# Kernel tuning notes

Measured on AMD Instinct MI355X. Metric: run time of the kernel, lower is better.

Reference implementation:

```python
import jax, jax.numpy as jnp
import numpy as np

B, T, D, H, O = 8, 16384, 256, 256, 256


def setup_inputs() -> dict:
    key = jax.random.key(0)
    ks = jax.random.split(key, 7)
    lim_d = 1.0 / np.sqrt(D)
    lim_h = 1.0 / np.sqrt(H)
    u = lambda k, shape, lim: jax.random.uniform(k, shape, jnp.float32, -lim, lim)
    return {
        "xs": jax.random.normal(ks[0], (B, T, D), jnp.float32),
        "Wz": u(ks[1], (H, D), lim_d),
        "bz": u(ks[2], (H,), lim_d),
        "Wh": u(ks[3], (H, D), lim_d),
        "bh": u(ks[4], (H,), lim_d),
        "Wo": u(ks[5], (O, H), lim_h),
        "bo": u(ks[6], (O,), lim_h),
    }


def reference(xs, Wz, bz, Wh, bh, Wo, bo):
    # gates and candidate hidden states (eqx.nn.Linear: y = W @ x + b)
    zs = jax.nn.sigmoid(jnp.einsum("btd,hd->bth", xs, Wz) + bz)  # [B,T,H]
    hs = jnp.einsum("btd,hd->bth", xs, Wh) + bh                  # [B,T,H]

    # prepend_ones / prepend_zeros along the time axis
    a = jnp.concatenate([jnp.ones_like(zs[:, :1]), 1.0 - zs], axis=1)    # [B,T+1,H]
    b = jnp.concatenate([jnp.zeros_like(zs[:, :1]), zs * hs], axis=1)    # [B,T+1,H]

    def combine(first, second):
        a0, b0 = first
        a1, b1 = second
        return (a0 * b0, b0 * a1 + b1)

    _, states = jax.lax.associative_scan(combine, (a, b), axis=1)
    return jnp.einsum("bth,oh->bto", states[:, 1:], Wo) + bo  # [B,T,O]
```

## Files before the change

### kernel.cpp

```cpp
#include <hip/hip_runtime.h>
#include <hip/hip_bf16.h>

#define Bsz 8
#define Tsz 16384
#define NL0 16385
#define NL5 512
#define NL10 16

typedef __attribute__((ext_vector_type(2))) float f32x2;
typedef __attribute__((ext_vector_type(4))) float f32x4;
typedef __attribute__((ext_vector_type(8))) short bf16x8;

__device__ __forceinline__ short f2bf(float f) {
  unsigned u = __builtin_bit_cast(unsigned, f);
  u += 0x7FFFu + ((u >> 16) & 1u);
  return (short)(u >> 16);
}
__device__ __forceinline__ unsigned cvtpk(float lo, float hi) {
  __hip_bfloat162 t = __float22bfloat162_rn(float2{lo, hi});
  unsigned u;
  __builtin_memcpy(&u, &t, 4);
  return u;
}
__device__ __forceinline__ bf16x8 pack8(f32x4 a, f32x4 b) {
  union { unsigned u[4]; bf16x8 v; } r;
  r.u[0] = cvtpk(a[0], a[1]); r.u[1] = cvtpk(a[2], a[3]);
  r.u[2] = cvtpk(b[0], b[1]); r.u[3] = cvtpk(b[2], b[3]);
  return r.v;
}
__device__ __forceinline__ void unpk(unsigned u, float& a, float& b) {
  a = __builtin_bit_cast(float, u << 16);
  b = __builtin_bit_cast(float, u & 0xFFFF0000u);
}

__global__ void fill_sentinel(float* __restrict__ out, int n) {
  int i = blockIdx.x * blockDim.x + threadIdx.x;
  if (i < n) out[i] = 12345.0f;
}

__global__ void prep_weights(const float* __restrict__ Wz, const float* __restrict__ Wh,
                             const float* __restrict__ Wo, unsigned short* __restrict__ wt) {
  int idx = blockIdx.x * 256 + threadIdx.x;
  if (idx >= 3 * 256 * 32) return;
  int m   = idx >> 13;
  int rem = idx & 8191;
  int r   = rem >> 5;
  int cq  = rem & 31;
  const float* src = (m == 0 ? Wz : (m == 1 ? Wh : Wo)) + r * 256 + cq * 8;
  f32x4 v0 = *(const f32x4*)src;
  f32x4 v1 = *(const f32x4*)(src + 4);
  *(bf16x8*)(wt + m * 65536 + (cq * 256 + r) * 8) = pack8(v0, v1);
}

__global__ void init_e0(unsigned* __restrict__ l0) {
  int idx = blockIdx.x * 256 + threadIdx.x;
  if (idx >= Bsz * 256) return;
  int batch = idx >> 8, h = idx & 255;
  l0[(size_t)batch * NL0 * 256 + h] = 0x00003F80u;
}

__global__ __launch_bounds__(512, 3)
void gemm_zh(const float* __restrict__ xs, const unsigned short* __restrict__ wt,
             const float* __restrict__ bz, const float* __restrict__ bh,
             unsigned* __restrict__ l0)
{
  __shared__ __align__(16) unsigned short aL[2][4096];

  const int tid = threadIdx.x;
  const int wave = tid >> 6, lane = tid & 63, l15 = lane & 15, l4 = lane >> 4;
  const int rowBase = blockIdx.x * 64;
  const int srow = tid & 63, soct = tid >> 6;
  const float* aptr = xs + (size_t)(rowBase + srow) * 256 + soct * 8;
  const unsigned short* wz_t = wt;
  const unsigned short* wh_t = wt + 65536;
  const int wn = wave * 32;

  f32x4 accz[4][2] = {};
  f32x4 acch[4][2] = {};

  f32x4 av0 = __builtin_nontemporal_load((const f32x4*)aptr);
  f32x4 av1 = __builtin_nontemporal_load((const f32x4*)(aptr + 4));
  *(bf16x8*)&aL[0][(soct * 64 + srow) * 8] = pack8(av0, av1);

  bf16x8 zc[2], hc[2], zn[2], hn[2];
#pragma unroll
  for (int n = 0; n < 2; ++n) {
    const int r = wn + n * 16 + l15;
    zc[n] = *(const bf16x8*)(wz_t + (l4 * 256 + r) * 8);
    hc[n] = *(const bf16x8*)(wh_t + (l4 * 256 + r) * 8);
  }

#pragma unroll
  for (int kk = 0; kk < 8; ++kk) {
    const int S = kk >> 1;
    if ((kk & 1) == 0) {
      __syncthreads();
      if (S < 3) {
        av0 = __builtin_nontemporal_load((const f32x4*)(aptr + (S + 1) * 64));
        av1 = __builtin_nontemporal_load((const f32x4*)(aptr + (S + 1) * 64 + 4));
      }
    }
    if (kk < 7) {
      const int cq = (kk + 1) * 4 + l4;
#pragma unroll
      for (int n = 0; n < 2; ++n) {
        const int r = wn + n * 16 + l15;
        zn[n] = *(const bf16x8*)(wz_t + (cq * 256 + r) * 8);
        hn[n] = *(const bf16x8*)(wh_t + (cq * 256 + r) * 8);
      }
    }
    bf16x8 af[4];
#pragma unroll
    for (int m = 0; m < 4; ++m)
      af[m] = *(const bf16x8*)&aL[S & 1][(((kk & 1) * 4 + l4) * 64 + m * 16 + l15) * 8];
#pragma unroll
    for (int m = 0; m < 4; ++m)
#pragma unroll
      for (int n = 0; n < 2; ++n) {
        accz[m][n] = __builtin_amdgcn_mfma_f32_16x16x32_bf16(af[m], zc[n], accz[m][n], 0, 0, 0);
        acch[m][n] = __builtin_amdgcn_mfma_f32_16x16x32_bf16(af[m], hc[n], acch[m][n], 0, 0, 0);
      }
    if ((kk & 1) && S < 3)
      *(bf16x8*)&aL[(S & 1) ^ 1][(soct * 64 + srow) * 8] = pack8(av0, av1);
    if (kk < 7) {
      zc[0] = zn[0]; zc[1] = zn[1];
      hc[0] = hn[0]; hc[1] = hn[1];
    }
  }

  const int batch = rowBase >> 14;
  const int tRow  = rowBase & (Tsz - 1);
#pragma unroll
  for (int n = 0; n < 2; ++n) {
    const int col = wn + n * 16 + l15;
    const float bzv = bz[col], bhv = bh[col];
#pragma unroll
    for (int m = 0; m < 4; ++m)
#pragma unroll
      for (int j = 0; j < 4; ++j) {
        const int t = tRow + m * 16 + l4 * 4 + j;
        const float zv = 1.0f / (1.0f + __expf(-(accz[m][n][j] + bzv)));
        const float hv = acch[m][n][j] + bhv;
        l0[((size_t)batch * NL0 + t + 1) * 256 + col] = cvtpk(1.0f - zv, zv * hv);
      }
  }
}

__global__ __launch_bounds__(256)
void chunk_up_bf16(const unsigned* __restrict__ l0, f32x2* __restrict__ dst)
{
  int idx = blockIdx.x * 256 + threadIdx.x;
  int h2 = idx & 127, r = idx >> 7;
  int c = r & 511, batch = r >> 9;
  size_t base = ((size_t)batch * NL0 + (size_t)c * 32) * 256 + h2 * 2;

  float ax[16], bx[16], ay[16], by[16];
#pragma unroll
  for (int i = 0; i < 16; ++i) {
    uint2 e0 = *(const uint2*)(l0 + base + (size_t)(2 * i) * 256);
    uint2 e1 = *(const uint2*)(l0 + base + (size_t)(2 * i + 1) * 256);
    float a0, b0, a1, b1;
    unpk(e0.x, a0, b0); unpk(e1.x, a1, b1);
    ax[i] = a0 * b0; bx[i] = b0 * a1 + b1;
    unpk(e0.y, a0, b0); unpk(e1.y, a1, b1);
    ay[i] = a0 * b0; by[i] = b0 * a1 + b1;
  }
#pragma unroll
  for (int n = 8; n >= 1; n >>= 1) {
#pragma unroll
    for (int i = 0; i < n; ++i) {
      float nax = ax[2*i] * bx[2*i], nbx = bx[2*i] * ax[2*i+1] + bx[2*i+1];
      float nay = ay[2*i] * by[2*i], nby = by[2*i] * ay[2*i+1] + by[2*i+1];
      ax[i] = nax; bx[i] = nbx; ay[i] = nay; by[i] = nby;
    }
  }
  f32x4 o = {ax[0], bx[0], ay[0], by[0]};
  *(f32x4*)((float*)dst + (((size_t)batch * 512 + c) * 256 + h2 * 2) * 2) = o;
}

__global__ __launch_bounds__(256)
void chunk_up(const f32x2* __restrict__ src, f32x2* __restrict__ dst, int nCh, int nSrc)
{
  int idx = blockIdx.x * 256 + threadIdx.x;
  int total = Bsz * nCh * 256;
  if (idx >= total) return;
  int h = idx & 255, r = idx >> 8;
  int c = r % nCh, batch = r / nCh;
  size_t base = ((size_t)batch * nSrc + (size_t)c * 32) * 256 + h;

  float a1[16], b1[16];
#pragma unroll
  for (int i = 0; i < 16; ++i) {
    f32x2 e0 = src[base + (size_t)(2 * i) * 256];
    f32x2 e1 = src[base + (size_t)(2 * i + 1) * 256];
    a1[i] = e0[0] * e0[1];
    b1[i] = e0[1] * e1[0] + e1[1];
  }
#pragma unroll
  for (int n = 8; n >= 1; n >>= 1) {
#pragma unroll
    for (int i = 0; i < n; ++i) {
      float na = a1[2 * i] * b1[2 * i];
      float nb = b1[2 * i] * a1[2 * i + 1] + b1[2 * i + 1];
      a1[i] = na; b1[i] = nb;
    }
  }
  dst[((size_t)batch * nCh + c) * 256 + h] = f32x2{a1[0], b1[0]};
}

__global__ void tree16(const f32x2* __restrict__ src, float* __restrict__ outB)
{
  int idx = blockIdx.x * 256 + threadIdx.x;
  if (idx >= Bsz * 256) return;
  int h = idx & 255, batch = idx >> 8;
  size_t base = (size_t)batch * 16 * 256 + h;

  float a0[16], b0[16];
#pragma unroll
  for (int i = 0; i < 16; ++i) { f32x2 e = src[base + (size_t)i * 256]; a0[i] = e[0]; b0[i] = e[1]; }
  float a1[8], b1[8];
#pragma unroll
  for (int i = 0; i < 8; ++i) { a1[i] = a0[2*i]*b0[2*i]; b1[i] = b0[2*i]*a0[2*i+1] + b0[2*i+1]; }
  float a2[4], b2[4];
#pragma unroll
  for (int i = 0; i < 4; ++i) { a2[i] = a1[2*i]*b1[2*i]; b2[i] = b1[2*i]*a1[2*i+1] + b1[2*i+1]; }
  float a3[2], b3[2];
#pragma unroll
  for (int i = 0; i < 2; ++i) { a3[i] = a2[2*i]*b2[2*i]; b3[i] = b2[2*i]*a2[2*i+1] + b2[2*i+1]; }
  float s3[2];
  s3[0] = b3[0];
  s3[1] = b3[0] * a3[1] + b3[1];
  float s2[4];
  s2[0] = b2[0]; s2[1] = s3[0]; s2[2] = s3[0] * a2[2] + b2[2]; s2[3] = s3[1];
  float s1[8];
  s1[0] = b1[0];
#pragma unroll
  for (int j = 0; j < 4; ++j) s1[2*j+1] = s2[j];
#pragma unroll
  for (int j = 1; j < 4; ++j) s1[2*j] = s2[j-1] * a1[2*j] + b1[2*j];
  float s0[16];
  s0[0] = b0[0];
#pragma unroll
  for (int j = 0; j < 8; ++j) s0[2*j+1] = s1[j];
#pragma unroll
  for (int j = 1; j < 8; ++j) s0[2*j] = s1[j-1] * a0[2*j] + b0[2*j];
#pragma unroll
  for (int i = 0; i < 16; ++i) outB[base + (size_t)i * 256] = s0[i];
}

__global__ __launch_bounds__(256, 2)
void chunk_down_f32(const f32x2* __restrict__ src, const float* __restrict__ snext,
                    float* __restrict__ outF, int nCh, int nFull, int nSrc)
{
  int idx = blockIdx.x * 256 + threadIdx.x;
  int total = Bsz * nCh * 256;
  if (idx >= total) return;
  int h = idx & 255, r = idx >> 8;
  int c = r % nCh, batch = r / nCh;
  size_t base = ((size_t)batch * nSrc + (size_t)c * 32) * 256 + h;
  bool hasP = (c > 0);
  float P = hasP ? snext[((size_t)batch * nFull + (c - 1)) * 256 + h] : 0.0f;
  float S = snext[((size_t)batch * nFull + c) * 256 + h];

  float ae[16], be[16], a1[16], b1[16];
#pragma unroll
  for (int i = 0; i < 16; ++i) {
    f32x2 e0 = src[base + (size_t)(2 * i) * 256];
    f32x2 e1 = src[base + (size_t)(2 * i + 1) * 256];
    ae[i] = e0[0]; be[i] = e0[1];
    a1[i] = e0[0] * e0[1];
    b1[i] = e0[1] * e1[0] + e1[1];
  }
  float a2[8], b2[8];
#pragma unroll
  for (int i = 0; i < 8; ++i) { a2[i] = a1[2*i]*b1[2*i]; b2[i] = b1[2*i]*a1[2*i+1] + b1[2*i+1]; }
  float a3[4], b3[4];
#pragma unroll
  for (int i = 0; i < 4; ++i) { a3[i] = a2[2*i]*b2[2*i]; b3[i] = b2[2*i]*a2[2*i+1] + b2[2*i+1]; }
  float a4[2], b4[2];
#pragma unroll
  for (int i = 0; i < 2; ++i) { a4[i] = a3[2*i]*b3[2*i]; b4[i] = b3[2*i]*a3[2*i+1] + b3[2*i+1]; }

  float s4[2];
  s4[0] = hasP ? P * a4[0] + b4[0] : b4[0];
  s4[1] = S;
  float s3[4];
  s3[0] = hasP ? P * a3[0] + b3[0] : b3[0];
  s3[1] = s4[0]; s3[2] = s4[0] * a3[2] + b3[2]; s3[3] = s4[1];
  float s2[8];
  s2[0] = hasP ? P * a2[0] + b2[0] : b2[0];
#pragma unroll
  for (int j = 0; j < 4; ++j) s2[2*j+1] = s3[j];
#pragma unroll
  for (int j = 1; j < 4; ++j) s2[2*j] = s3[j-1] * a2[2*j] + b2[2*j];
  float s1[16];
  s1[0] = hasP ? P * a1[0] + b1[0] : b1[0];
#pragma unroll
  for (int j = 0; j < 8; ++j) s1[2*j+1] = s2[j];
#pragma unroll
  for (int j = 1; j < 8; ++j) s1[2*j] = s2[j-1] * a1[2*j] + b1[2*j];

  outF[base] = hasP ? P * ae[0] + be[0] : be[0];
#pragma unroll
  for (int j = 0; j < 16; ++j) outF[base + (size_t)(2*j+1) * 256] = s1[j];
#pragma unroll
  for (int j = 1; j < 16; ++j) outF[base + (size_t)(2*j) * 256] = s1[j-1] * ae[j] + be[j];
}

__global__ __launch_bounds__(256, 2)
void down_proj(const unsigned* __restrict__ l0, const float* __restrict__ s5b,
               const unsigned short* __restrict__ wo_t, const float* __restrict__ bo,
               float* __restrict__ out)
{
  __shared__ unsigned short pL[32 * 256];

  const int tid = threadIdx.x;
  const int bc = blockIdx.x;
  const int c = bc % 513;
  const int batch = bc / 513;

  {
    const int h = tid;
    const size_t base = ((size_t)batch * NL0 + (size_t)c * 32) * 256 + h;
    const bool hasP = (c > 0);
    const float P = hasP ? s5b[((size_t)batch * 512 + (c - 1)) * 256 + h] : 0.0f;

    if (c == 512) {
      float a0, b0; unpk(__builtin_nontemporal_load(l0 + base), a0, b0);
      pL[h] = (unsigned short)f2bf(P * a0 + b0);
#pragma unroll
      for (int i = 1; i < 32; ++i)
        pL[i * 256 + (h ^ ((i & 7) << 3))] = 0;
    } else {
      const float S = s5b[((size_t)batch * 512 + c) * 256 + h];
      float ae[16], be[16], a1[16], b1[16];
#pragma unroll
      for (int i = 0; i < 16; ++i) {
        unsigned u0 = __builtin_nontemporal_load(l0 + base + (size_t)(2 * i) * 256);
        unsigned u1 = __builtin_nontemporal_load(l0 + base + (size_t)(2 * i + 1) * 256);
        float a0, b0, a1e, b1e;
        unpk(u0, a0, b0); unpk(u1, a1e, b1e);
        ae[i] = a0; be[i] = b0;
        a1[i] = a0 * b0; b1[i] = b0 * a1e + b1e;
      }
      float a2[8], b2[8];
#pragma unroll
      for (int i = 0; i < 8; ++i) { a2[i] = a1[2*i]*b1[2*i]; b2[i] = b1[2*i]*a1[2*i+1] + b1[2*i+1]; }
      float a3[4], b3[4];
#pragma unroll
      for (int i = 0; i < 4; ++i) { a3[i] = a2[2*i]*b2[2*i]; b3[i] = b2[2*i]*a2[2*i+1] + b2[2*i+1]; }
      float a4[2], b4[2];
#pragma unroll
      for (int i = 0; i < 2; ++i) { a4[i] = a3[2*i]*b3[2*i]; b4[i] = b3[2*i]*a3[2*i+1] + b3[2*i+1]; }

      float s4[2];
      s4[0] = hasP ? P * a4[0] + b4[0] : b4[0];
      s4[1] = S;
      float s3[4];
      s3[0] = hasP ? P * a3[0] + b3[0] : b3[0];
      s3[1] = s4[0]; s3[2] = s4[0] * a3[2] + b3[2]; s3[3] = s4[1];
      float s2[8];
      s2[0] = hasP ? P * a2[0] + b2[0] : b2[0];
#pragma unroll
      for (int j = 0; j < 4; ++j) s2[2*j+1] = s3[j];
#pragma unroll
      for (int j = 1; j < 4; ++j) s2[2*j] = s3[j-1] * a2[2*j] + b2[2*j];
      float s1[16];
      s1[0] = hasP ? P * a1[0] + b1[0] : b1[0];
#pragma unroll
      for (int j = 0; j < 8; ++j) s1[2*j+1] = s2[j];
#pragma unroll
      for (int j = 1; j < 8; ++j) s1[2*j] = s2[j-1] * a1[2*j] + b1[2*j];

      pL[h] = (unsigned short)f2bf(hasP ? P * ae[0] + be[0] : be[0]);
#pragma unroll
      for (int j = 0; j < 16; ++j) {
        const int row = 2 * j + 1;
        pL[row * 256 + (h ^ ((row & 7) << 3))] = (unsigned short)f2bf(s1[j]);
      }
#pragma unroll
      for (int j = 1; j < 16; ++j) {
        const int row = 2 * j;
        pL[row * 256 + (h ^ ((row & 7) << 3))] = (unsigned short)f2bf(s1[j-1] * ae[j] + be[j]);
      }
    }
  }
  __syncthreads();

  const int wave = tid >> 6, lane = tid & 63, l15 = lane & 15, l4 = lane >> 4;
  const int wn = wave * 64;
  f32x4 acc[2][4] = {};
  bf16x8 wc[4], wnx[4];
#pragma unroll
  for (int n = 0; n < 4; ++n)
    wc[n] = *(const bf16x8*)(wo_t + (l4 * 256 + wn + n * 16 + l15) * 8);
#pragma unroll
  for (int kk = 0; kk < 8; ++kk) {
    if (kk < 7) {
#pragma unroll
      for (int n = 0; n < 4; ++n)
        wnx[n] = *(const bf16x8*)(wo_t + (((kk + 1) * 4 + l4) * 256 + wn + n * 16 + l15) * 8);
    }
    bf16x8 af[2];
#pragma unroll
    for (int m = 0; m < 2; ++m) {
      const int row = m * 16 + l15;
      af[m] = *(const bf16x8*)&pL[row * 256 + ((kk * 32 + l4 * 8) ^ ((row & 7) << 3))];
    }
#pragma unroll
    for (int m = 0; m < 2; ++m)
#pragma unroll
      for (int n = 0; n < 4; ++n)
        acc[m][n] = __builtin_amdgcn_mfma_f32_16x16x32_bf16(af[m], wc[n], acc[m][n], 0, 0, 0);
    if (kk < 7) {
      wc[0] = wnx[0]; wc[1] = wnx[1]; wc[2] = wnx[2]; wc[3] = wnx[3];
    }
  }

  const int tBase = 32 * c - 1;
#pragma unroll
  for (int n = 0; n < 4; ++n) {
    const int col = wn + n * 16 + l15;
    const float bv = bo[col];
#pragma unroll
    for (int m = 0; m < 2; ++m)
#pragma unroll
      for (int j = 0; j < 4; ++j) {
        const int t = tBase + m * 16 + l4 * 4 + j;
        if ((unsigned)t < (unsigned)Tsz)
          __builtin_nontemporal_store(acc[m][n][j] + bv,
                                      &out[((size_t)batch * Tsz + t) * 256 + col]);
      }
  }
}

extern "C" void kernel_launch(void* const* d_in, const int* in_sizes, int n_in,
                              void* d_out, int out_size, void* d_ws, size_t ws_size,
                              hipStream_t stream)
{
  (void)in_sizes; (void)n_in;
  const float* xs = (const float*)d_in[0];
  const float* Wz = (const float*)d_in[1];
  const float* bz = (const float*)d_in[2];
  const float* Wh = (const float*)d_in[3];
  const float* bh = (const float*)d_in[4];
  const float* Wo = (const float*)d_in[5];
  const float* bo = (const float*)d_in[6];
  float* out = (float*)d_out;

  const size_t n_l0  = (size_t)Bsz * NL0 * 256;
  const size_t n_l5  = (size_t)Bsz * NL5 * 256;
  const size_t n_l10 = (size_t)Bsz * NL10 * 256;

  unsigned* l0    = (unsigned*)d_ws;
  f32x2* l5ab     = (f32x2*)(l0 + n_l0);
  f32x2* l10ab    = l5ab + n_l5;
  float* s10b     = (float*)(l10ab + n_l10);
  float* s5b      = s10b + n_l10;
  unsigned short* wt = (unsigned short*)(s5b + n_l5);

  const size_t need = n_l0 * 4 + n_l5 * 8 + n_l10 * 8 + n_l10 * 4 + n_l5 * 4 + 3 * 65536 * 2;
  if (ws_size < need) {
    fill_sentinel<<<(out_size + 255) / 256, 256, 0, stream>>>(out, out_size);
    return;
  }

  prep_weights<<<96, 256, 0, stream>>>(Wz, Wh, Wo, wt);
  init_e0<<<8, 256, 0, stream>>>(l0);
  gemm_zh<<<Bsz * Tsz / 64, 512, 0, stream>>>(xs, wt, bz, bh, l0);

  chunk_up_bf16<<<(Bsz * 512 * 128) / 256, 256, 0, stream>>>(l0, l5ab);
  chunk_up<<<(Bsz * 16 * 256) / 256, 256, 0, stream>>>(l5ab, l10ab, 16, NL5);
  tree16<<<8, 256, 0, stream>>>(l10ab, s10b);
  chunk_down_f32<<<(Bsz * 16 * 256) / 256, 256, 0, stream>>>(l5ab, s10b, s5b, 16, 16, NL5);

  down_proj<<<Bsz * 513, 256, 0, stream>>>(l0, s5b, wt + 2 * 65536, bo, out);
}
```

Baseline: 199.7 us.

## Stage full A tile in LDS upfront and drop nontemporal hints

```diff
diff --git a/kernel.cpp b/kernel.cpp
--- a/kernel.cpp
+++ b/kernel.cpp
@@ -59,12 +59,12 @@
   l0[(size_t)batch * NL0 * 256 + h] = 0x00003F80u;
 }
 
-__global__ __launch_bounds__(512, 3)
+__global__ __launch_bounds__(512, 4)
 void gemm_zh(const float* __restrict__ xs, const unsigned short* __restrict__ wt,
              const float* __restrict__ bz, const float* __restrict__ bh,
              unsigned* __restrict__ l0)
 {
-  __shared__ __align__(16) unsigned short aL[2][4096];
+  __shared__ __align__(16) unsigned short aL[32][64][8];
 
   const int tid = threadIdx.x;
   const int wave = tid >> 6, lane = tid & 63, l15 = lane & 15, l4 = lane >> 4;
@@ -75,12 +75,21 @@
   const unsigned short* wh_t = wt + 65536;
   const int wn = wave * 32;
 
+  {
+    f32x4 avA[4], avB[4];
+#pragma unroll
+    for (int q = 0; q < 4; ++q) {
+      avA[q] = *(const f32x4*)(aptr + q * 64);
+      avB[q] = *(const f32x4*)(aptr + q * 64 + 4);
+    }
+#pragma unroll
+    for (int q = 0; q < 4; ++q)
+      *(bf16x8*)&aL[soct + q * 8][srow][0] = pack8(avA[q], avB[q]);
+  }
+  __syncthreads();
+
   f32x4 accz[4][2] = {};
   f32x4 acch[4][2] = {};
-
-  f32x4 av0 = __builtin_nontemporal_load((const f32x4*)aptr);
-  f32x4 av1 = __builtin_nontemporal_load((const f32x4*)(aptr + 4));
-  *(bf16x8*)&aL[0][(soct * 64 + srow) * 8] = pack8(av0, av1);
 
   bf16x8 zc[2], hc[2], zn[2], hn[2];
 #pragma unroll
@@ -92,14 +101,6 @@
 
 #pragma unroll
   for (int kk = 0; kk < 8; ++kk) {
-    const int S = kk >> 1;
-    if ((kk & 1) == 0) {
-      __syncthreads();
-      if (S < 3) {
-        av0 = __builtin_nontemporal_load((const f32x4*)(aptr + (S + 1) * 64));
-        av1 = __builtin_nontemporal_load((const f32x4*)(aptr + (S + 1) * 64 + 4));
-      }
-    }
     if (kk < 7) {
       const int cq = (kk + 1) * 4 + l4;
 #pragma unroll
@@ -112,7 +113,7 @@
     bf16x8 af[4];
 #pragma unroll
     for (int m = 0; m < 4; ++m)
-      af[m] = *(const bf16x8*)&aL[S & 1][(((kk & 1) * 4 + l4) * 64 + m * 16 + l15) * 8];
+      af[m] = *(const bf16x8*)&aL[kk * 4 + l4][m * 16 + l15][0];
 #pragma unroll
     for (int m = 0; m < 4; ++m)
 #pragma unroll
@@ -120,8 +121,6 @@
         accz[m][n] = __builtin_amdgcn_mfma_f32_16x16x32_bf16(af[m], zc[n], accz[m][n], 0, 0, 0);
         acch[m][n] = __builtin_amdgcn_mfma_f32_16x16x32_bf16(af[m], hc[n], acch[m][n], 0, 0, 0);
       }
-    if ((kk & 1) && S < 3)
-      *(bf16x8*)&aL[(S & 1) ^ 1][(soct * 64 + srow) * 8] = pack8(av0, av1);
     if (kk < 7) {
       zc[0] = zn[0]; zc[1] = zn[1];
       hc[0] = hn[0]; hc[1] = hn[1];
@@ -326,7 +325,7 @@
     const float P = hasP ? s5b[((size_t)batch * 512 + (c - 1)) * 256 + h] : 0.0f;
 
     if (c == 512) {
-      float a0, b0; unpk(__builtin_nontemporal_load(l0 + base), a0, b0);
+      float a0, b0; unpk(l0[base], a0, b0);
       pL[h] = (unsigned short)f2bf(P * a0 + b0);
 #pragma unroll
       for (int i = 1; i < 32; ++i)
@@ -336,8 +335,8 @@
       float ae[16], be[16], a1[16], b1[16];
 #pragma unroll
       for (int i = 0; i < 16; ++i) {
-        unsigned u0 = __builtin_nontemporal_load(l0 + base + (size_t)(2 * i) * 256);
-        unsigned u1 = __builtin_nontemporal_load(l0 + base + (size_t)(2 * i + 1) * 256);
+        unsigned u0 = l0[base + (size_t)(2 * i) * 256];
+        unsigned u1 = l0[base + (size_t)(2 * i + 1) * 256];
         float a0, b0, a1e, b1e;
         unpk(u0, a0, b0); unpk(u1, a1e, b1e);
         ae[i] = a0; be[i] = b0;
@@ -428,8 +427,7 @@
       for (int j = 0; j < 4; ++j) {
         const int t = tBase + m * 16 + l4 * 4 + j;
         if ((unsigned)t < (unsigned)Tsz)
-          __builtin_nontemporal_store(acc[m][n][j] + bv,
-                                      &out[((size_t)batch * Tsz + t) * 256 + col]);
+          out[((size_t)batch * Tsz + t) * 256 + col] = acc[m][n][j] + bv;
       }
   }
 }
```

After: 186.4 us. 1.07x faster.
